# Kernel tuning notes

Measured on AMD Instinct MI355X. Metric: run time of the kernel, lower is better.

## Reference

```python
import jax, jax.numpy as jnp
import numpy as np


def setup_inputs() -> dict:
    key = jax.random.key(0)
    k1, k2 = jax.random.split(key)
    L, B, H = 1024, 64, 1024
    encoder_outputs = jax.random.normal(k1, (L, B, H), dtype=jnp.float32)
    decoder_gru_out = jax.random.normal(k2, (1, B, H), dtype=jnp.float32)
    return {"encoder_outputs": encoder_outputs, "decoder_gru_out": decoder_gru_out}


def reference(encoder_outputs, decoder_gru_out):
    # scores[l,b] = sum_h enc[l,b,h] * dec[0,b,h]
    scores = jnp.einsum('lbh,bh->lb', encoder_outputs, decoder_gru_out[0])
    # softmax over the sequence (L) axis
    attn = jax.nn.softmax(scores, axis=0)  # [L, B]
    # context[b,h] = sum_l attn[l,b] * enc[l,b,h]
    context = jnp.einsum('lb,lbh->bh', attn, encoder_outputs)
    return context
```

## Files before the change

kernel.cpp:

```cpp
#include <hip/hip_runtime.h>
#include <math.h>

#define L_SEQ 1024
#define BATCH 64
#define HDIM  1024
#define WPB   4

#define LOG2E 1.44269504088896340736f

template <int SPLIT, int CHUNK>
__global__ __launch_bounds__(256, 4) void attn_partial_kernel(
    const float* __restrict__ enc, const float* __restrict__ dec,
    float* __restrict__ wsC, float* __restrict__ wsML)
{
    constexpr int NG = CHUNK / 2;
    const int tid  = threadIdx.x;
    const int lane = tid & 63;
    const int wave = tid >> 6;
    const int w    = blockIdx.x * WPB + wave;
    const int b    = w / SPLIT;
    const int k    = w - b * SPLIT;
    const int l0   = k * CHUNK;

    const float4* decv = (const float4*)(dec + (size_t)b * HDIM);
    float4 d[4];
    #pragma unroll
    for (int q = 0; q < 4; ++q) d[q] = decv[lane + 64 * q];

    float m = -INFINITY;
    float lsum = 0.0f;
    float4 a[4];
    #pragma unroll
    for (int q = 0; q < 4; ++q) a[q] = make_float4(0.f, 0.f, 0.f, 0.f);

    const size_t row_stride = (size_t)BATCH * HDIM;
    const float* base0 = enc + ((size_t)l0 * BATCH + b) * HDIM;

    float4 R[2][2][4];

    #pragma unroll
    for (int r = 0; r < 2; ++r) {
        const float4* row = (const float4*)(base0 + r * row_stride);
        #pragma unroll
        for (int q = 0; q < 4; ++q) R[0][r][q] = row[lane + 64 * q];
    }

    #pragma unroll
    for (int g = 0; g < NG; ++g) {
        const int buf = g & 1;

        if (g + 1 < NG) {
            const float* nbase = base0 + (size_t)(2 * (g + 1)) * row_stride;
            #pragma unroll
            for (int r = 0; r < 2; ++r) {
                const float4* row = (const float4*)(nbase + r * row_stride);
                #pragma unroll
                for (int q = 0; q < 4; ++q) R[buf ^ 1][r][q] = row[lane + 64 * q];
            }
        }

        float p0 = 0.0f, p1 = 0.0f;
        #pragma unroll
        for (int q = 0; q < 4; ++q) {
            p0 = fmaf(R[buf][0][q].x, d[q].x, p0);
            p0 = fmaf(R[buf][0][q].y, d[q].y, p0);
            p0 = fmaf(R[buf][0][q].z, d[q].z, p0);
            p0 = fmaf(R[buf][0][q].w, d[q].w, p0);
            p1 = fmaf(R[buf][1][q].x, d[q].x, p1);
            p1 = fmaf(R[buf][1][q].y, d[q].y, p1);
            p1 = fmaf(R[buf][1][q].z, d[q].z, p1);
            p1 = fmaf(R[buf][1][q].w, d[q].w, p1);
        }

        #pragma unroll
        for (int off = 32; off > 0; off >>= 1) {
            p0 += __shfl_xor(p0, off, 64);
            p1 += __shfl_xor(p1, off, 64);
        }

        const float s0 = p0 * LOG2E;
        const float s1 = p1 * LOG2E;
        const float gm = fmaxf(s0, s1);

        if (gm > m) {
            const float scale = exp2f(m - gm);
            lsum *= scale;
            #pragma unroll
            for (int q = 0; q < 4; ++q) {
                a[q].x *= scale;  a[q].y *= scale;
                a[q].z *= scale;  a[q].w *= scale;
            }
            m = gm;
        }

        const float w0 = exp2f(s0 - m);
        const float w1 = exp2f(s1 - m);
        lsum += w0 + w1;
        #pragma unroll
        for (int q = 0; q < 4; ++q) {
            a[q].x = fmaf(w1, R[buf][1][q].x, fmaf(w0, R[buf][0][q].x, a[q].x));
            a[q].y = fmaf(w1, R[buf][1][q].y, fmaf(w0, R[buf][0][q].y, a[q].y));
            a[q].z = fmaf(w1, R[buf][1][q].z, fmaf(w0, R[buf][0][q].z, a[q].z));
            a[q].w = fmaf(w1, R[buf][1][q].w, fmaf(w0, R[buf][0][q].w, a[q].w));
        }
    }

    const size_t r = (size_t)b * SPLIT + k;
    float4* C = (float4*)(wsC + r * (size_t)HDIM);
    #pragma unroll
    for (int q = 0; q < 4; ++q) C[lane + 64 * q] = a[q];
    if (lane == 0) {
        wsML[2 * r]     = m;
        wsML[2 * r + 1] = lsum;
    }
}

__global__ __launch_bounds__(256) void attn_reduce_kernel(
    const float* __restrict__ wsC, const float* __restrict__ wsML,
    float* __restrict__ out, int split)
{
    const int b = blockIdx.x >> 2;
    const int q = blockIdx.x & 3;
    const int h = q * 256 + threadIdx.x;

    float M = -INFINITY;
    for (int k = 0; k < split; ++k)
        M = fmaxf(M, wsML[2 * ((size_t)b * split + k)]);

    float Ltot = 0.0f;
    float acc = 0.0f;
    for (int k = 0; k < split; ++k) {
        const size_t r = (size_t)b * split + k;
        const float wgt = exp2f(wsML[2 * r] - M);
        Ltot = fmaf(wsML[2 * r + 1], wgt, Ltot);
        acc = fmaf(wsC[r * (size_t)HDIM + h], wgt, acc);
    }
    out[(size_t)b * HDIM + h] = acc / Ltot;
}

extern "C" void kernel_launch(void* const* d_in, const int* in_sizes, int n_in,
                              void* d_out, int out_size, void* d_ws, size_t ws_size,
                              hipStream_t stream) {
    const float* enc = (const float*)d_in[0];
    const float* dec = (const float*)d_in[1];
    float* out = (float*)d_out;

    const size_t need128 = (size_t)BATCH * 128 * HDIM * sizeof(float)
                         + (size_t)BATCH * 128 * 2 * sizeof(float);
    float* wsC = (float*)d_ws;

    if (ws_size >= need128) {
        constexpr int SPLIT = 128, CHUNK = L_SEQ / 128;
        float* wsML = wsC + (size_t)BATCH * SPLIT * HDIM;
        attn_partial_kernel<SPLIT, CHUNK>
            <<<(BATCH * SPLIT) / WPB, 256, 0, stream>>>(enc, dec, wsC, wsML);
        attn_reduce_kernel<<<BATCH * 4, 256, 0, stream>>>(wsC, wsML, out, SPLIT);
    } else {
        constexpr int SPLIT = 16, CHUNK = L_SEQ / 16;
        float* wsML = wsC + (size_t)BATCH * SPLIT * HDIM;
        attn_partial_kernel<SPLIT, CHUNK>
            <<<(BATCH * SPLIT) / WPB, 256, 0, stream>>>(enc, dec, wsC, wsML);
        attn_reduce_kernel<<<BATCH * 4, 256, 0, stream>>>(wsC, wsML, out, SPLIT);
    }
}
```

Before: 401.3 us.

## Process rows one at a time with staggered prefetch and halve L split

Restructures the partial kernel's inner loop. It now processes one encoder row at a time with two alternating register buffers, issuing each row's load before computing the previous row, instead of double-buffering pairs of rows. This cuts register pressure, and the min-occupancy launch bound is dropped. The sequence split per batch goes from 128 to 64 (fallback 16 to 8), which halves workspace traffic and reduce-kernel work but launches fewer waves with longer serial chunks.

```diff
diff --git a/kernel.cpp b/kernel.cpp
--- a/kernel.cpp
+++ b/kernel.cpp
@@ -9,11 +9,10 @@
 #define LOG2E 1.44269504088896340736f
 
 template <int SPLIT, int CHUNK>
-__global__ __launch_bounds__(256, 4) void attn_partial_kernel(
+__global__ __launch_bounds__(256) void attn_partial_kernel(
     const float* __restrict__ enc, const float* __restrict__ dec,
     float* __restrict__ wsC, float* __restrict__ wsML)
 {
-    constexpr int NG = CHUNK / 2;
     const int tid  = threadIdx.x;
     const int lane = tid & 63;
     const int wave = tid >> 6;
@@ -36,73 +35,62 @@
     const size_t row_stride = (size_t)BATCH * HDIM;
     const float* base0 = enc + ((size_t)l0 * BATCH + b) * HDIM;
 
-    float4 R[2][2][4];
-
-    #pragma unroll
-    for (int r = 0; r < 2; ++r) {
-        const float4* row = (const float4*)(base0 + r * row_stride);
-        #pragma unroll
-        for (int q = 0; q < 4; ++q) R[0][r][q] = row[lane + 64 * q];
-    }
-
-    #pragma unroll
-    for (int g = 0; g < NG; ++g) {
-        const int buf = g & 1;
-
-        if (g + 1 < NG) {
-            const float* nbase = base0 + (size_t)(2 * (g + 1)) * row_stride;
-            #pragma unroll
-            for (int r = 0; r < 2; ++r) {
-                const float4* row = (const float4*)(nbase + r * row_stride);
-                #pragma unroll
-                for (int q = 0; q < 4; ++q) R[buf ^ 1][r][q] = row[lane + 64 * q];
-            }
-        }
-
-        float p0 = 0.0f, p1 = 0.0f;
+    float4 B0[4], B1[4];
+    auto process = [&](const float4* e) {
+        float p = 0.0f;
         #pragma unroll
         for (int q = 0; q < 4; ++q) {
-            p0 = fmaf(R[buf][0][q].x, d[q].x, p0);
-            p0 = fmaf(R[buf][0][q].y, d[q].y, p0);
-            p0 = fmaf(R[buf][0][q].z, d[q].z, p0);
-            p0 = fmaf(R[buf][0][q].w, d[q].w, p0);
-            p1 = fmaf(R[buf][1][q].x, d[q].x, p1);
-            p1 = fmaf(R[buf][1][q].y, d[q].y, p1);
-            p1 = fmaf(R[buf][1][q].z, d[q].z, p1);
-            p1 = fmaf(R[buf][1][q].w, d[q].w, p1);
+            p = fmaf(e[q].x, d[q].x, p);
+            p = fmaf(e[q].y, d[q].y, p);
+            p = fmaf(e[q].z, d[q].z, p);
+            p = fmaf(e[q].w, d[q].w, p);
         }
+        #pragma unroll
+        for (int off = 32; off > 0; off >>= 1)
+            p += __shfl_xor(p, off, 64);
 
-        #pragma unroll
-        for (int off = 32; off > 0; off >>= 1) {
-            p0 += __shfl_xor(p0, off, 64);
-            p1 += __shfl_xor(p1, off, 64);
-        }
-
-        const float s0 = p0 * LOG2E;
-        const float s1 = p1 * LOG2E;
-        const float gm = fmaxf(s0, s1);
-
-        if (gm > m) {
-            const float scale = exp2f(m - gm);
+        const float s = p * LOG2E;
+        if (s > m) {
+            const float scale = exp2f(m - s);
             lsum *= scale;
             #pragma unroll
             for (int q = 0; q < 4; ++q) {
                 a[q].x *= scale;  a[q].y *= scale;
                 a[q].z *= scale;  a[q].w *= scale;
             }
-            m = gm;
+            m = s;
         }
-
-        const float w0 = exp2f(s0 - m);
-        const float w1 = exp2f(s1 - m);
-        lsum += w0 + w1;
+        const float wgt = exp2f(s - m);
+        lsum += wgt;
         #pragma unroll
         for (int q = 0; q < 4; ++q) {
-            a[q].x = fmaf(w1, R[buf][1][q].x, fmaf(w0, R[buf][0][q].x, a[q].x));
-            a[q].y = fmaf(w1, R[buf][1][q].y, fmaf(w0, R[buf][0][q].y, a[q].y));
-            a[q].z = fmaf(w1, R[buf][1][q].z, fmaf(w0, R[buf][0][q].z, a[q].z));
-            a[q].w = fmaf(w1, R[buf][1][q].w, fmaf(w0, R[buf][0][q].w, a[q].w));
+            a[q].x = fmaf(wgt, e[q].x, a[q].x);
+            a[q].y = fmaf(wgt, e[q].y, a[q].y);
+            a[q].z = fmaf(wgt, e[q].z, a[q].z);
+            a[q].w = fmaf(wgt, e[q].w, a[q].w);
         }
+    };
+
+    {
+        const float4* row = (const float4*)base0;
+        #pragma unroll
+        for (int q = 0; q < 4; ++q) B0[q] = row[lane + 64 * q];
+    }
+
+    #pragma unroll
+    for (int g = 0; g < CHUNK; g += 2) {
+        {
+            const float4* row = (const float4*)(base0 + (size_t)(g + 1) * row_stride);
+            #pragma unroll
+            for (int q = 0; q < 4; ++q) B1[q] = row[lane + 64 * q];
+        }
+        process(B0);
+        if (g + 2 < CHUNK) {
+            const float4* row = (const float4*)(base0 + (size_t)(g + 2) * row_stride);
+            #pragma unroll
+            for (int q = 0; q < 4; ++q) B0[q] = row[lane + 64 * q];
+        }
+        process(B1);
     }
 
     const size_t r = (size_t)b * SPLIT + k;
@@ -145,18 +133,18 @@
     const float* dec = (const float*)d_in[1];
     float* out = (float*)d_out;
 
-    const size_t need128 = (size_t)BATCH * 128 * HDIM * sizeof(float)
-                         + (size_t)BATCH * 128 * 2 * sizeof(float);
+    const size_t need64 = (size_t)BATCH * 64 * HDIM * sizeof(float)
+                        + (size_t)BATCH * 64 * 2 * sizeof(float);
     float* wsC = (float*)d_ws;
 
-    if (ws_size >= need128) {
-        constexpr int SPLIT = 128, CHUNK = L_SEQ / 128;
+    if (ws_size >= need64) {
+        constexpr int SPLIT = 64, CHUNK = L_SEQ / 64;
         float* wsML = wsC + (size_t)BATCH * SPLIT * HDIM;
         attn_partial_kernel<SPLIT, CHUNK>
             <<<(BATCH * SPLIT) / WPB, 256, 0, stream>>>(enc, dec, wsC, wsML);
         attn_reduce_kernel<<<BATCH * 4, 256, 0, stream>>>(wsC, wsML, out, SPLIT);
     } else {
-        constexpr int SPLIT = 16, CHUNK = L_SEQ / 16;
+        constexpr int SPLIT = 8, CHUNK = L_SEQ / 8;
         float* wsML = wsC + (size_t)BATCH * SPLIT * HDIM;
         attn_partial_kernel<SPLIT, CHUNK>
             <<<(BATCH * SPLIT) / WPB, 256, 0, stream>>>(enc, dec, wsC, wsML);
```

Result: faster. 379.3 us (-5.5%).
